# Optimization experiments

Measured on AMD Instinct MI355X. Metric: run time of the kernel, lower is better.

## Reference

```python
import jax, jax.numpy as jnp
from jax import lax
import numpy as np

GROUPS = 32

def setup_inputs() -> dict:
    key = jax.random.key(0)
    ks = jax.random.split(key, 12)
    B, C, H, O, N = 4, 256, 256, 256, 4096
    s = 0.02  # small init scale to keep logits in a stable range
    x  = jax.random.normal(ks[0], (B, C, N), dtype=jnp.float32)
    Wk = jax.random.normal(ks[1], (H, C), dtype=jnp.float32) * s
    bk = jax.random.normal(ks[2], (H,), dtype=jnp.float32) * s
    Wq = jax.random.normal(ks[3], (H, C), dtype=jnp.float32) * s
    bq = jax.random.normal(ks[4], (H,), dtype=jnp.float32) * s
    W1 = jax.random.normal(ks[5], (H, C), dtype=jnp.float32) * s
    b1 = jax.random.normal(ks[6], (H,), dtype=jnp.float32) * s
    # grouped conv1d kernel: (out_ch, in_ch // groups, kw) in 'OIH' layout
    W2 = jax.random.normal(ks[7], (H, H // GROUPS, 3), dtype=jnp.float32) * s
    b2 = jax.random.normal(ks[8], (H,), dtype=jnp.float32) * s
    W3 = jax.random.normal(ks[9], (O, H), dtype=jnp.float32) * s
    b3 = jax.random.normal(ks[10], (O,), dtype=jnp.float32) * s
    return {"x": x, "Wk": Wk, "bk": bk, "Wq": Wq, "bq": bq,
            "W1": W1, "b1": b1, "W2": W2, "b2": b2, "W3": W3, "b3": b3}


def reference(x, Wk, bk, Wq, bq, W1, b1, W2, b2, W3, b3):
    # k: 1x1 conv then permute(0,2,1) -> [B, N, H]
    k = jnp.einsum('hc,bcn->bnh', Wk, x) + bk
    # q: 1x1 conv -> [B, H, N]
    q = jnp.einsum('hc,bcn->bhn', Wq, x) + bq[None, :, None]
    # sim = softmax(k @ q, dim=-2): softmax over the FIRST N axis (rows)
    sim = jax.nn.softmax(jnp.einsum('bnh,bhm->bnm', k, q), axis=-2)  # [B, N, N]
    # v path: 1x1 conv -> grouped 3-tap conv (pad=1) -> ReLU -> 1x1 conv
    v1 = jnp.einsum('hc,bcn->bhn', W1, x) + b1[None, :, None]
    v2 = lax.conv_general_dilated(
        v1, W2, window_strides=(1,), padding='SAME',
        feature_group_count=GROUPS,
        dimension_numbers=('NCH', 'OIH', 'NCH')) + b2[None, :, None]
    v2 = jax.nn.relu(v2)
    v = jnp.einsum('oh,bhn->bon', W3, v2) + b3[None, :, None]  # [B, O, N]
    # out = v @ sim -> [B, O, N]
    return jnp.einsum('bon,bnm->bom', v, sim)
```

## Files before the change

### kernel.cpp

```cpp
#include <hip/hip_runtime.h>


#define B_ 4
#define C_ 256
#define H_ 256
#define O_ 256
#define N_ 4096
#define NSPLIT 4
#define SPAN (N_ / NSPLIT)
#define ITERS (SPAN / 32)

typedef short short8 __attribute__((ext_vector_type(8)));
typedef float floatx4 __attribute__((ext_vector_type(4)));
typedef float floatx16 __attribute__((ext_vector_type(16)));
typedef unsigned uint2v __attribute__((ext_vector_type(2)));

__device__ __forceinline__ unsigned short f2bf(float f) {
  unsigned u = __float_as_uint(f);
  u = (u + 0x7fffu + ((u >> 16) & 1u)) >> 16;
  return (unsigned short)u;
}
__device__ __forceinline__ float bf2f(unsigned short u) {
  return __uint_as_float(((unsigned)u) << 16);
}
__device__ __forceinline__ floatx4 mfma16(short8 a, short8 b, floatx4 c) {
  return __builtin_amdgcn_mfma_f32_16x16x32_bf16(a, b, c, 0, 0, 0);
}
__device__ __forceinline__ floatx16 mfma32(short8 a, short8 b, floatx16 c) {
  return __builtin_amdgcn_mfma_f32_32x32x16_bf16(a, b, c, 0, 0, 0);
}
__device__ __forceinline__ unsigned pack2bf(float a, float b) {
  return __builtin_amdgcn_perm(__float_as_uint(b) + 0x8000u,
                               __float_as_uint(a) + 0x8000u, 0x07060302u);
}

__global__ __launch_bounds__(256) void prep_transpose_kernel(
    const float* __restrict__ x, unsigned short* __restrict__ xt,
    const float* __restrict__ Wk, const float* __restrict__ Wq,
    const float* __restrict__ W1, const float* __restrict__ W3,
    unsigned short* __restrict__ wk, unsigned short* __restrict__ wq,
    unsigned short* __restrict__ w1, unsigned short* __restrict__ w3) {
  __shared__ unsigned short tile[64][66];
  const int gid = blockIdx.x;
  const int t = threadIdx.x;
  if (gid >= 1024) {
    const int i = (gid - 1024) * 256 + t;
    wk[i] = f2bf(Wk[i]);
    wq[i] = f2bf(Wq[i]);
    w1[i] = f2bf(W1[i]);
    w3[i] = f2bf(W3[i]);
    return;
  }
  const int b  = gid >> 8;
  const int ct = (gid >> 6) & 3;
  const int nt = gid & 63;
  const int c0 = ct * 64, n0 = nt * 64;
  const float* xb = x + ((size_t)b * C_ + c0) * N_ + n0;
#pragma unroll
  for (int rr = 0; rr < 4; ++rr) {
    const int c = (t >> 4) + rr * 16;
    const floatx4 v = *reinterpret_cast<const floatx4*>(
        xb + (size_t)c * N_ + (t & 15) * 4);
#pragma unroll
    for (int i = 0; i < 4; ++i) tile[c][(t & 15) * 4 + i] = f2bf(v[i]);
  }
  __syncthreads();
  unsigned short* xo = xt + ((size_t)b * N_ + n0) * C_ + c0;
#pragma unroll
  for (int rr = 0; rr < 2; ++rr) {
    const int nr = (t >> 3) + rr * 32;
    short8 pk;
#pragma unroll
    for (int i = 0; i < 8; ++i) pk[i] = (short)tile[(t & 7) * 8 + i][nr];
    *reinterpret_cast<short8*>(xo + (size_t)nr * C_ + (t & 7) * 8) = pk;
  }
}

__global__ __launch_bounds__(256) void gemm1_kernel(
    const unsigned short* __restrict__ xt,
    const unsigned short* __restrict__ wk, const unsigned short* __restrict__ wq,
    const unsigned short* __restrict__ w1,
    const float* __restrict__ bk, const float* __restrict__ bq,
    const float* __restrict__ b1,
    unsigned short* __restrict__ ko, unsigned short* __restrict__ qo,
    unsigned short* __restrict__ v1o) {
  const int lane = threadIdx.x & 63;
  const int wid  = blockIdx.x * 4 + (threadIdx.x >> 6);
  const int b  = wid >> 9;
  const int r  = wid & 511;
  const int hh = r >> 8;
  const int nt = r & 255;
  const int n0 = nt * 16;
  const int m  = lane & 15;
  const int q  = lane >> 4;

  const unsigned short* xrow = xt + ((size_t)(b * N_) + n0 + m) * C_;
  const unsigned short* Ws[3] = {wk, wq, w1};

  floatx4 acc[3][8];
  const floatx4 z = {0.f, 0.f, 0.f, 0.f};
#pragma unroll
  for (int o = 0; o < 3; ++o)
#pragma unroll
    for (int tt = 0; tt < 8; ++tt) acc[o][tt] = z;

  for (int cs = 0; cs < 8; ++cs) {
    const int cb = cs * 32 + q * 8;
    short8 af = *reinterpret_cast<const short8*>(xrow + cb);
#pragma unroll
    for (int o = 0; o < 3; ++o) {
#pragma unroll
      for (int tt = 0; tt < 8; ++tt) {
        const int h0 = (hh * 8 + tt) * 16;
        short8 bf = *reinterpret_cast<const short8*>(Ws[o] + (h0 + m) * C_ + cb);
        acc[o][tt] = mfma16(af, bf, acc[o][tt]);
      }
    }
  }

#pragma unroll
  for (int tt = 0; tt < 8; ++tt) {
    const int ks16 = hh * 8 + tt;
    const float bias = bk[ks16 * 16 + m];
#pragma unroll
    for (int r2 = 0; r2 < 4; ++r2) {
      const int n = n0 + q * 4 + r2;
      ko[((size_t)(b * 128 + (n >> 5))) * 8192 + ks16 * 512 + (m >> 3) * 256 +
         (n & 31) * 8 + (m & 7)] = f2bf(acc[0][tt][r2] + bias);
    }
  }
  const float* biases[2] = {bq, b1};
  unsigned short* outs[2] = {qo, v1o};
#pragma unroll
  for (int o = 0; o < 2; ++o) {
#pragma unroll
    for (int tt = 0; tt < 8; ++tt) {
      const int h0 = (hh * 8 + tt) * 16;
      const float bias = biases[o][h0 + m];
#pragma unroll
      for (int r2 = 0; r2 < 4; ++r2) {
        const int n = n0 + q * 4 + r2;
        outs[o][(b * N_ + n) * H_ + h0 + m] = f2bf(acc[o + 1][tt][r2] + bias);
      }
    }
  }
}

__global__ __launch_bounds__(256) void convgemm2_kernel(
    const unsigned short* __restrict__ v1, const float* __restrict__ W2,
    const float* __restrict__ b2, const unsigned short* __restrict__ w3,
    const float* __restrict__ b3, unsigned short* __restrict__ vo) {
  __shared__ unsigned short v2L[32][264];

  const int h   = threadIdx.x;
  const int blk = blockIdx.x;
  const int b   = blk >> 7;
  const int nc  = blk & 127;
  const int n0  = nc * 32;
  const int g8  = h & ~7;

  {
    float w[24];
#pragma unroll
    for (int i = 0; i < 24; ++i) w[i] = W2[h * 24 + i];
    const float bias = b2[h];
    const unsigned short* vb = v1 + (size_t)b * (N_ * H_) + g8;

    float fp[8], fc[8], fn[8];
    if (n0 == 0) {
#pragma unroll
      for (int i = 0; i < 8; ++i) fp[i] = 0.f;
    } else {
      short8 u = *reinterpret_cast<const short8*>(vb + (size_t)(n0 - 1) * H_);
#pragma unroll
      for (int i = 0; i < 8; ++i) fp[i] = bf2f((unsigned short)u[i]);
    }
    {
      short8 u = *reinterpret_cast<const short8*>(vb + (size_t)n0 * H_);
#pragma unroll
      for (int i = 0; i < 8; ++i) fc[i] = bf2f((unsigned short)u[i]);
    }
#pragma unroll 1
    for (int ns = 0; ns < 32; ++ns) {
      const int n = n0 + ns;
      if (n + 1 < N_) {
        short8 u = *reinterpret_cast<const short8*>(vb + (size_t)(n + 1) * H_);
#pragma unroll
        for (int i = 0; i < 8; ++i) fn[i] = bf2f((unsigned short)u[i]);
      } else {
#pragma unroll
        for (int i = 0; i < 8; ++i) fn[i] = 0.f;
      }
      float a = bias;
#pragma unroll
      for (int i = 0; i < 8; ++i)
        a += w[i * 3] * fp[i] + w[i * 3 + 1] * fc[i] + w[i * 3 + 2] * fn[i];
      v2L[ns][h] = f2bf(fmaxf(a, 0.f));
#pragma unroll
      for (int i = 0; i < 8; ++i) { fp[i] = fc[i]; fc[i] = fn[i]; }
    }
  }
  __syncthreads();

  const int ln = threadIdx.x & 63;
  const int wv = threadIdx.x >> 6;
  const int m  = ln & 31;
  const int hl = ln >> 5;

  floatx16 acc2[2];
#pragma unroll
  for (int ot = 0; ot < 2; ++ot)
#pragma unroll
    for (int r = 0; r < 16; ++r) acc2[ot][r] = 0.f;

#pragma unroll
  for (int ks = 0; ks < 16; ++ks) {
    short8 bfr = *reinterpret_cast<const short8*>(&v2L[m][ks * 16 + hl * 8]);
#pragma unroll
    for (int ot = 0; ot < 2; ++ot) {
      const int o0 = wv * 64 + ot * 32;
      short8 afr = *reinterpret_cast<const short8*>(
          w3 + (o0 + m) * H_ + ks * 16 + hl * 8);
      acc2[ot] = mfma32(afr, bfr, acc2[ot]);
    }
  }

  const int kn = (m >> 4) & 1;
  const int nl = m & 15;
  unsigned short* vkn = vo + ((size_t)(b * 128 + nc) * 2 + kn) * 4096;
#pragma unroll
  for (int ot = 0; ot < 2; ++ot)
#pragma unroll
    for (int r = 0; r < 16; ++r) {
      const int o = wv * 64 + ot * 32 + (r & 3) + 8 * (r >> 2) + 4 * hl;
      vkn[(o >> 5) * 512 + (nl >> 3) * 256 + (o & 31) * 8 + (nl & 7)] =
          f2bf(acc2[ot][r] + b3[o]);
    }
}

__global__ __launch_bounds__(512, 2) void attn_kernel(
    const unsigned short* __restrict__ kbf, const unsigned short* __restrict__ qbf,
    const unsigned short* __restrict__ vbf,
    unsigned short* __restrict__ pacc, float* __restrict__ pml) {
  __shared__ __attribute__((aligned(16))) char smem[6][16384];

  const int tid = threadIdx.x;
  const int ln  = tid & 63;
  const int wv  = tid >> 6;
  const int gid = blockIdx.x;
  const int b   = gid & 3;
  const int s   = (gid >> 2) & 3;
  const int mt256 = gid >> 4;
  const int mt32  = mt256 * 8 + wv;
  const int m0  = mt32 * 32;
  const int m   = ln & 31;
  const int hl  = ln >> 5;
  const int lane_base = ln * 16;

  const unsigned short* qrow = qbf + ((size_t)b * N_ + m0 + m) * H_ + hl * 8;
  short8 qf[16];
#pragma unroll
  for (int ks = 0; ks < 16; ++ks)
    qf[ks] = *reinterpret_cast<const short8*>(qrow + ks * 16);

  floatx16 acc[8];
#pragma unroll
  for (int t = 0; t < 8; ++t)
#pragma unroll
    for (int r = 0; r < 16; ++r) acc[t][r] = 0.f;
  float Lp = 0.f;

  const size_t row0 = (size_t)(b * 128 + s * 32);

  auto stage = [&](int slot, int nc) {
    const char* kg = (const char*)(kbf + (row0 + nc) * 8192);
    const char* vg = (const char*)(vbf + (row0 + nc) * 8192);
    char* lk = &smem[slot][0];
    char* lv = &smem[3 + slot][0];
#pragma unroll
    for (int j = 0; j < 2; ++j) {
      const int ofs = j * 8192 + tid * 16;
      __builtin_amdgcn_global_load_lds(
          (const __attribute__((address_space(1))) void*)(kg + ofs),
          (__attribute__((address_space(3))) void*)(lk + ofs), 16, 0, 0);
      __builtin_amdgcn_global_load_lds(
          (const __attribute__((address_space(1))) void*)(vg + ofs),
          (__attribute__((address_space(3))) void*)(lv + ofs), 16, 0, 0);
    }
  };

  stage(0, 0);
  stage(1, 1);

  int cur = 0;
#pragma unroll 1
  for (int nc = 0; nc < ITERS; ++nc) {
    if (nc + 1 < ITERS) {
      asm volatile("s_waitcnt vmcnt(4)\n\ts_barrier" ::: "memory");
    } else {
      asm volatile("s_waitcnt vmcnt(0)\n\ts_barrier" ::: "memory");
    }
    __builtin_amdgcn_sched_barrier(0);
    if (nc + 2 < ITERS) {
      int ps = cur + 2; if (ps >= 3) ps -= 3;
      stage(ps, nc + 2);
    }

    const char* sk = &smem[cur][0];
    const char* sv = &smem[3 + cur][0];

    floatx16 sacc;
#pragma unroll
    for (int r = 0; r < 16; ++r) sacc[r] = 0.f;
    __builtin_amdgcn_s_setprio(1);
#pragma unroll
    for (int ks = 0; ks < 16; ++ks) {
      short8 kf = *reinterpret_cast<const short8*>(sk + lane_base + ks * 1024);
      sacc = mfma32(kf, qf[ks], sacc);
    }
    __builtin_amdgcn_s_setprio(0);

    short8 pf0, pf1;
#if __has_builtin(__builtin_amdgcn_permlane32_swap)
    unsigned d[8];
#pragma unroll
    for (int i = 0; i < 8; ++i) {
      const float a = __expf(sacc[2 * i]);
      const float bb = __expf(sacc[2 * i + 1]);
      Lp += a + bb;
      d[i] = pack2bf(a, bb);
    }
#pragma unroll
    for (int g = 0; g < 2; ++g) {
      uint2v r0 = __builtin_amdgcn_permlane32_swap(d[4 * g + 0], d[4 * g + 2],
                                                   false, false);
      uint2v r1 = __builtin_amdgcn_permlane32_swap(d[4 * g + 1], d[4 * g + 3],
                                                   false, false);
      d[4 * g + 0] = r0.x; d[4 * g + 2] = r0.y;
      d[4 * g + 1] = r1.x; d[4 * g + 3] = r1.y;
    }
    union { unsigned u[4]; short8 s8; } c0, c1;
    c0.u[0] = d[0]; c0.u[1] = d[1]; c0.u[2] = d[2]; c0.u[3] = d[3];
    c1.u[0] = d[4]; c1.u[1] = d[5]; c1.u[2] = d[6]; c1.u[3] = d[7];
    pf0 = c0.s8;
    pf1 = c1.s8;
#else
    float pv[16];
#pragma unroll
    for (int r = 0; r < 16; ++r) { pv[r] = __expf(sacc[r]); Lp += pv[r]; }
    unsigned wpk[8];
#pragma unroll
    for (int r4 = 0; r4 < 4; ++r4) {
      wpk[r4]     = pack2bf(pv[r4], pv[r4 + 4]);
      wpk[r4 + 4] = pack2bf(pv[r4 + 8], pv[r4 + 12]);
    }
    const int hlsh = hl * 16;
#pragma unroll
    for (int j = 0; j < 8; ++j) {
      const int srcLane = m + ((j >> 2) << 5);
      const int u0 = __shfl((int)wpk[j & 3],       srcLane);
      const int u1 = __shfl((int)wpk[(j & 3) + 4], srcLane);
      pf0[j] = (short)((unsigned)u0 >> hlsh);
      pf1[j] = (short)((unsigned)u1 >> hlsh);
    }
#endif

    __builtin_amdgcn_s_setprio(1);
#pragma unroll
    for (int ot = 0; ot < 8; ++ot) {
      short8 vf0 = *reinterpret_cast<const short8*>(sv + lane_base + ot * 1024);
      short8 vf1 = *reinterpret_cast<const short8*>(
          sv + lane_base + 8192 + ot * 1024);
      acc[ot] = mfma32(vf0, pf0, acc[ot]);
      acc[ot] = mfma32(vf1, pf1, acc[ot]);
    }
    __builtin_amdgcn_s_setprio(0);

    cur = (cur == 2) ? 0 : cur + 1;
  }

  float Lv = Lp + __shfl_xor(Lp, 32);
  const float invL = 1.f / Lv;

  const int pwid = (b * 128 + mt32) * NSPLIT + s;
  unsigned short* pa = pacc + (size_t)pwid * (O_ * 32);
#pragma unroll
  for (int ot = 0; ot < 8; ++ot)
#pragma unroll
    for (int r = 0; r < 16; ++r) {
      const int o = ot * 32 + (r & 3) + 8 * (r >> 2) + 4 * hl;
      pa[o * 32 + m] = f2bf(acc[ot][r] * invL);
    }
  if (hl == 0) pml[pwid * 32 + m] = Lv;
}

__global__ __launch_bounds__(256) void combine_kernel(
    const unsigned short* __restrict__ pacc, const float* __restrict__ pml,
    float* __restrict__ out) {
  const int blk = blockIdx.x;
  const int b   = blk >> 7;
  const int mw  = blk & 127;
  const int o   = threadIdx.x;
  const int base = (b * 128 + mw) * NSPLIT;

  __shared__ float w[NSPLIT][32];
  if (threadIdx.x < 32) {
    const int c = threadIdx.x;
    float L[NSPLIT], sum = 0.f;
#pragma unroll
    for (int sp = 0; sp < NSPLIT; ++sp) {
      L[sp] = pml[(base + sp) * 32 + c];
      sum += L[sp];
    }
    const float inv = 1.f / sum;
#pragma unroll
    for (int sp = 0; sp < NSPLIT; ++sp) w[sp][c] = L[sp] * inv;
  }
  __syncthreads();

  float res[32];
#pragma unroll
  for (int c = 0; c < 32; ++c) res[c] = 0.f;
#pragma unroll
  for (int sp = 0; sp < NSPLIT; ++sp) {
    const unsigned short* pa =
        pacc + (size_t)(base + sp) * (O_ * 32) + o * 32;
#pragma unroll
    for (int c8 = 0; c8 < 4; ++c8) {
      short8 u = *reinterpret_cast<const short8*>(pa + c8 * 8);
#pragma unroll
      for (int i = 0; i < 8; ++i)
        res[c8 * 8 + i] =
            fmaf(w[sp][c8 * 8 + i], bf2f((unsigned short)u[i]), res[c8 * 8 + i]);
    }
  }
  float* ob = out + ((size_t)(b * O_ + o)) * N_ + mw * 32;
#pragma unroll
  for (int c4 = 0; c4 < 8; ++c4) {
    floatx4 v4 = {res[c4 * 4], res[c4 * 4 + 1], res[c4 * 4 + 2], res[c4 * 4 + 3]};
    *reinterpret_cast<floatx4*>(ob + c4 * 4) = v4;
  }
}

extern "C" void kernel_launch(void* const* d_in, const int* in_sizes, int n_in,
                              void* d_out, int out_size, void* d_ws, size_t ws_size,
                              hipStream_t stream) {
  const float* x  = (const float*)d_in[0];
  const float* Wk = (const float*)d_in[1];
  const float* bk = (const float*)d_in[2];
  const float* Wq = (const float*)d_in[3];
  const float* bq = (const float*)d_in[4];
  const float* W1 = (const float*)d_in[5];
  const float* b1 = (const float*)d_in[6];
  const float* W2 = (const float*)d_in[7];
  const float* b2 = (const float*)d_in[8];
  const float* W3 = (const float*)d_in[9];
  const float* b3 = (const float*)d_in[10];
  float* out = (float*)d_out;

  char* ws = (char*)d_ws;
  const size_t SZ = (size_t)B_ * N_ * H_ * sizeof(unsigned short);
  unsigned short* wkbf = (unsigned short*)(ws);
  unsigned short* wqbf = (unsigned short*)(ws + 131072);
  unsigned short* w1bf = (unsigned short*)(ws + 262144);
  unsigned short* w3bf = (unsigned short*)(ws + 393216);
  char* base = ws + 524288;
  unsigned short* kbf  = (unsigned short*)(base);
  unsigned short* qbf  = (unsigned short*)(base + SZ);
  unsigned short* vbf  = (unsigned short*)(base + 2 * SZ);
  unsigned short* xtbf = (unsigned short*)(base + 3 * SZ);
  unsigned short* v1bf = (unsigned short*)(base + 4 * SZ);
  unsigned short* pacc = (unsigned short*)(base + 3 * SZ);
  float*          pml  = (float*)(base + 7 * SZ);

  prep_transpose_kernel<<<1280, 256, 0, stream>>>(
      x, xtbf, Wk, Wq, W1, W3, wkbf, wqbf, w1bf, w3bf);
  gemm1_kernel<<<512, 256, 0, stream>>>(xtbf, wkbf, wqbf, w1bf, bk, bq, b1,
                                        kbf, qbf, v1bf);
  convgemm2_kernel<<<512, 256, 0, stream>>>(v1bf, W2, b2, w3bf, b3, vbf);
  attn_kernel<<<256, 512, 0, stream>>>(kbf, qbf, vbf, pacc, pml);
  combine_kernel<<<512, 256, 0, stream>>>(pacc, pml, out);
}
```

Baseline: 248.7 us.

## Stagger half the waves to run PV one chunk behind QK for MFMA overlap

Waves 4-7 now run the PV matmul for the previous chunk before the QK and softmax for the current one, while waves 0-3 keep the original order. The aim is to interleave MFMA-heavy and exp/permute-heavy phases across waves so the matrix cores stay busier. V staging grows from 3 to 4 LDS slots so the lagging group still has its chunk resident, which raises shared memory from 96KB to 112KB per block. That may limit the two-blocks-per-CU occupancy the launch bounds request.

```diff
diff --git a/kernel.cpp b/kernel.cpp
--- a/kernel.cpp
+++ b/kernel.cpp
@@ -242,7 +242,7 @@
     const unsigned short* __restrict__ kbf, const unsigned short* __restrict__ qbf,
     const unsigned short* __restrict__ vbf,
     unsigned short* __restrict__ pacc, float* __restrict__ pml) {
-  __shared__ __attribute__((aligned(16))) char smem[6][16384];
+  __shared__ __attribute__((aligned(16))) char smem[7][16384];
 
   const int tid = threadIdx.x;
   const int ln  = tid & 63;
@@ -255,6 +255,7 @@
   const int m0  = mt32 * 32;
   const int m   = ln & 31;
   const int hl  = ln >> 5;
+  const bool grpB = (wv >= 4);
   const int lane_base = ln * 16;
 
   const unsigned short* qrow = qbf + ((size_t)b * N_ + m0 + m) * H_ + hl * 8;
@@ -272,11 +273,11 @@
 
   const size_t row0 = (size_t)(b * 128 + s * 32);
 
-  auto stage = [&](int slot, int nc) {
+  auto stage = [&](int nc) {
     const char* kg = (const char*)(kbf + (row0 + nc) * 8192);
     const char* vg = (const char*)(vbf + (row0 + nc) * 8192);
-    char* lk = &smem[slot][0];
-    char* lv = &smem[3 + slot][0];
+    char* lk = &smem[nc % 3][0];
+    char* lv = &smem[3 + (nc & 3)][0];
 #pragma unroll
     for (int j = 0; j < 2; ++j) {
       const int ofs = j * 8192 + tid * 16;
@@ -289,26 +290,9 @@
     }
   };
 
-  stage(0, 0);
-  stage(1, 1);
-
-  int cur = 0;
-#pragma unroll 1
-  for (int nc = 0; nc < ITERS; ++nc) {
-    if (nc + 1 < ITERS) {
-      asm volatile("s_waitcnt vmcnt(4)\n\ts_barrier" ::: "memory");
-    } else {
-      asm volatile("s_waitcnt vmcnt(0)\n\ts_barrier" ::: "memory");
-    }
-    __builtin_amdgcn_sched_barrier(0);
-    if (nc + 2 < ITERS) {
-      int ps = cur + 2; if (ps >= 3) ps -= 3;
-      stage(ps, nc + 2);
-    }
-
-    const char* sk = &smem[cur][0];
-    const char* sv = &smem[3 + cur][0];
-
+  short8 pf0, pf1;
+
+  auto qk = [&](const char* sk) -> floatx16 {
     floatx16 sacc;
 #pragma unroll
     for (int r = 0; r < 16; ++r) sacc[r] = 0.f;
@@ -319,8 +303,21 @@
       sacc = mfma32(kf, qf[ks], sacc);
     }
     __builtin_amdgcn_s_setprio(0);
-
-    short8 pf0, pf1;
+    return sacc;
+  };
+  auto pv = [&](const char* sv) {
+    __builtin_amdgcn_s_setprio(1);
+#pragma unroll
+    for (int ot = 0; ot < 8; ++ot) {
+      short8 vf0 = *reinterpret_cast<const short8*>(sv + lane_base + ot * 1024);
+      short8 vf1 = *reinterpret_cast<const short8*>(
+          sv + lane_base + 8192 + ot * 1024);
+      acc[ot] = mfma32(vf0, pf0, acc[ot]);
+      acc[ot] = mfma32(vf1, pf1, acc[ot]);
+    }
+    __builtin_amdgcn_s_setprio(0);
+  };
+  auto softmax = [&](floatx16 sacc) {
 #if __has_builtin(__builtin_amdgcn_permlane32_swap)
     unsigned d[8];
 #pragma unroll
@@ -345,14 +342,14 @@
     pf0 = c0.s8;
     pf1 = c1.s8;
 #else
-    float pv[16];
-#pragma unroll
-    for (int r = 0; r < 16; ++r) { pv[r] = __expf(sacc[r]); Lp += pv[r]; }
+    float pv_[16];
+#pragma unroll
+    for (int r = 0; r < 16; ++r) { pv_[r] = __expf(sacc[r]); Lp += pv_[r]; }
     unsigned wpk[8];
 #pragma unroll
     for (int r4 = 0; r4 < 4; ++r4) {
-      wpk[r4]     = pack2bf(pv[r4], pv[r4 + 4]);
-      wpk[r4 + 4] = pack2bf(pv[r4 + 8], pv[r4 + 12]);
+      wpk[r4]     = pack2bf(pv_[r4], pv_[r4 + 4]);
+      wpk[r4 + 4] = pack2bf(pv_[r4 + 8], pv_[r4 + 12]);
     }
     const int hlsh = hl * 16;
 #pragma unroll
@@ -364,20 +361,34 @@
       pf1[j] = (short)((unsigned)u1 >> hlsh);
     }
 #endif
-
-    __builtin_amdgcn_s_setprio(1);
-#pragma unroll
-    for (int ot = 0; ot < 8; ++ot) {
-      short8 vf0 = *reinterpret_cast<const short8*>(sv + lane_base + ot * 1024);
-      short8 vf1 = *reinterpret_cast<const short8*>(
-          sv + lane_base + 8192 + ot * 1024);
-      acc[ot] = mfma32(vf0, pf0, acc[ot]);
-      acc[ot] = mfma32(vf1, pf1, acc[ot]);
-    }
-    __builtin_amdgcn_s_setprio(0);
-
-    cur = (cur == 2) ? 0 : cur + 1;
-  }
+  };
+
+  stage(0);
+  stage(1);
+
+#pragma unroll 1
+  for (int nc = 0; nc < ITERS; ++nc) {
+    if (nc + 1 < ITERS) {
+      asm volatile("s_waitcnt vmcnt(4)\n\ts_barrier" ::: "memory");
+    } else {
+      asm volatile("s_waitcnt vmcnt(0)\n\ts_barrier" ::: "memory");
+    }
+    __builtin_amdgcn_sched_barrier(0);
+    if (nc + 2 < ITERS) stage(nc + 2);
+
+    const char* sk = &smem[nc % 3][0];
+
+    if (!grpB) {
+      floatx16 sacc = qk(sk);
+      softmax(sacc);
+      pv(&smem[3 + (nc & 3)][0]);
+    } else {
+      if (nc > 0) pv(&smem[3 + ((nc - 1) & 3)][0]);
+      floatx16 sacc = qk(sk);
+      softmax(sacc);
+    }
+  }
+  if (grpB) pv(&smem[3 + ((ITERS - 1) & 3)][0]);
 
   float Lv = Lp + __shfl_xor(Lp, 32);
   const float invL = 1.f / Lv;
```

Result: faster. 242.5 us (-2.5%).
